# Optimization experiments

Hardware: AMD Instinct MI355X
Metric: run time of the kernel (lower is better)

Reference implementation:

```python
import jax, jax.numpy as jnp
import numpy as np

P = 50000      # number of graph nodes (cortical dipoles)
HID = 256      # hidden width
E = 800000     # number of nonzeros in Ahat (avg degree 16)


def setup_inputs() -> dict:
    key = jax.random.key(0)
    ks = jax.random.split(key, 12)
    beta = jax.random.normal(ks[0], (P, 1), dtype=jnp.float32)
    degree = jax.random.uniform(ks[1], (P, 1), dtype=jnp.float32)
    A_rows = jax.random.randint(ks[2], (E,), 0, P, dtype=jnp.int32)
    A_cols = jax.random.randint(ks[3], (E,), 0, P, dtype=jnp.int32)
    # normalized-adjacency-like positive values
    A_vals = jax.random.uniform(ks[4], (E,), dtype=jnp.float32) * (1.0 / 16.0)
    # parameters (torch nn.Linear stores weight as [out, in])
    s_in = 1.0 / np.sqrt(3.0)
    s_h = 1.0 / np.sqrt(HID)
    W_in = jax.random.uniform(ks[5], (HID, 3), jnp.float32, -s_in, s_in)
    b_in = jax.random.uniform(ks[6], (HID,), jnp.float32, -s_in, s_in)
    W_mp1 = jax.random.uniform(ks[7], (HID, HID), jnp.float32, -s_h, s_h)
    W_mp2 = jax.random.uniform(ks[8], (HID, HID), jnp.float32, -s_h, s_h)
    W_out = jax.random.uniform(ks[9], (1, HID), jnp.float32, -s_h, s_h)
    b_out = jax.random.uniform(ks[10], (1,), jnp.float32, -s_h, s_h)
    return {
        "beta": beta, "degree": degree,
        "A_rows": A_rows, "A_cols": A_cols, "A_vals": A_vals,
        "W_in": W_in, "b_in": b_in,
        "W_mp1": W_mp1, "W_mp2": W_mp2,
        "W_out": W_out, "b_out": b_out,
    }


def _spmm(A_rows, A_cols, A_vals, X):
    # sparse [P,P] @ dense [P,H] via gather + segment-sum over COO edges
    msgs = A_vals[:, None] * X[A_cols]            # [E, H]
    return jax.ops.segment_sum(msgs, A_rows, num_segments=P)


def reference(beta, degree, A_rows, A_cols, A_vals,
              W_in, b_in, W_mp1, W_mp2, W_out, b_out):
    x = jnp.concatenate([beta, beta ** 2, degree], axis=1)   # [P, 3]
    h = jax.nn.relu(x @ W_in.T + b_in)                       # [P, HID]
    AH = _spmm(A_rows, A_cols, A_vals, h)                    # one-hop
    A2H = _spmm(A_rows, A_cols, A_vals, AH)                  # two-hop
    h = jax.nn.relu(AH @ W_mp1.T + A2H @ W_mp2.T)            # fused sum + relu
    g = jax.nn.softplus(h @ W_out.T + b_out)                 # [P, 1]
    return g
```

## Files before the change

kernel.cpp:

```cpp
#include <hip/hip_runtime.h>
#include <math.h>

#define NP 50000
#define HIDDEN 256
#define NE 800000
#define CAP 64

#define OFF_X2     0ULL
#define OFF_BP     51200000ULL
#define OFF_CNT    51462144ULL
#define OFF_PC     51662144ULL
#define OFF_EV     52062144ULL

typedef __attribute__((ext_vector_type(8))) short bf16x8;
typedef __attribute__((ext_vector_type(8))) unsigned short u16x8;
typedef __attribute__((ext_vector_type(4))) float f32x4;

__device__ inline unsigned short f2bf(float f) {
    union { float f; unsigned int u; } x; x.f = f;
    unsigned int r = x.u + 0x7FFFu + ((x.u >> 16) & 1u);
    return (unsigned short)(r >> 16);
}
__device__ inline float bf2f(unsigned short u) {
    union { unsigned int u; float f; } x; x.u = ((unsigned int)u) << 16; return x.f;
}

__global__ void bp_kernel(const float* __restrict__ W1,
                          const float* __restrict__ W2,
                          unsigned short* __restrict__ Bp) {
    int t = blockIdx.x * 256 + threadIdx.x;
    int j = t >> 9;
    int k = t & 511;
    float v = (k < 256) ? W1[j * 256 + k] : W2[j * 256 + (k - 256)];
    Bp[(k >> 3) * 2048 + j * 8 + (k & 7)] = f2bf(v);
}

__global__ void pc_kernel(const float* __restrict__ beta,
                          const float* __restrict__ degree,
                          float2* __restrict__ pc) {
    int i = blockIdx.x * 256 + threadIdx.x;
    if (i < NP) pc[i] = make_float2(beta[i], degree[i]);
}

__global__ void scatter_ell(const int* __restrict__ rows,
                            const int* __restrict__ cols,
                            const float* __restrict__ vals,
                            int* __restrict__ cnt,
                            int2* __restrict__ ev) {
    int e = blockIdx.x * 256 + threadIdx.x;
    if (e < NE) {
        int r = rows[e];
        int pos = atomicAdd(&cnt[r], 1);
        if (pos < CAP)
            ev[(size_t)r * CAP + pos] = make_int2(cols[e], __float_as_int(vals[e]));
    }
}

__global__ __launch_bounds__(256) void spmm_embed_kernel(
        const int* __restrict__ cnt, const int2* __restrict__ ev,
        const float2* __restrict__ pc,
        const float* __restrict__ W_in, const float* __restrict__ b_in,
        unsigned short* __restrict__ Y, int ystride) {
    int w = threadIdx.x >> 6;
    int lane = threadIdx.x & 63;
    int r = blockIdx.x * 4 + w;
    if (r >= NP) return;
    int half = lane >> 5;
    int fo = (lane & 31) * 8;

    int n = min(cnt[r], CAP);
    int2 e2 = make_int2(0, 0);
    if (lane < n) e2 = ev[(size_t)r * CAP + lane];
    int col_l = e2.x;
    float val_l = __int_as_float(e2.y);

    float wr0[8], wr1[8], wr2[8], br[8];
    #pragma unroll
    for (int j = 0; j < 8; ++j) {
        wr0[j] = W_in[(fo + j) * 3 + 0];
        wr1[j] = W_in[(fo + j) * 3 + 1];
        wr2[j] = W_in[(fo + j) * 3 + 2];
        br[j]  = b_in[fo + j];
    }

    float acc[8] = {0.f,0.f,0.f,0.f,0.f,0.f,0.f,0.f};
    for (int i = 0; i < n; i += 8) {
        float2 p[4]; float vv[4];
        #pragma unroll
        for (int k = 0; k < 4; ++k) {
            int e = i + 2 * k + half;
            int es = (e < n) ? e : 0;
            int c = __shfl(col_l, es);
            vv[k] = __shfl(val_l, es);
            if (e >= n) vv[k] = 0.f;
            p[k] = pc[c];
        }
        #pragma unroll
        for (int k = 0; k < 4; ++k) {
            float b = p[k].x, d = p[k].y, v = vv[k];
            float b2 = b * b;
            #pragma unroll
            for (int j = 0; j < 8; ++j) {
                float t = fmaf(b, wr0[j], fmaf(b2, wr1[j], fmaf(d, wr2[j], br[j])));
                acc[j] = fmaf(v, fmaxf(t, 0.f), acc[j]);
            }
        }
    }
    #pragma unroll
    for (int j = 0; j < 8; ++j) acc[j] += __shfl_xor(acc[j], 32);
    if (half == 0) {
        u16x8 o;
        #pragma unroll
        for (int j = 0; j < 8; ++j) o[j] = f2bf(acc[j]);
        *reinterpret_cast<u16x8*>(Y + (size_t)r * ystride + fo) = o;
    }
}

__global__ __launch_bounds__(256) void spmm_gather_kernel(
        const int* __restrict__ cnt, const int2* __restrict__ ev,
        const unsigned short* __restrict__ X, int xstride,
        unsigned short* __restrict__ Y, int ystride) {
    int w = threadIdx.x >> 6;
    int lane = threadIdx.x & 63;
    int r = blockIdx.x * 4 + w;
    if (r >= NP) return;
    int half = lane >> 5;
    int fo = (lane & 31) * 8;

    int n = min(cnt[r], CAP);
    int2 e2 = make_int2(0, 0);
    if (lane < n) e2 = ev[(size_t)r * CAP + lane];
    int col_l = e2.x;
    float val_l = __int_as_float(e2.y);

    float acc[8] = {0.f,0.f,0.f,0.f,0.f,0.f,0.f,0.f};
    for (int i = 0; i < n; i += 8) {
        int cc[4]; float vv[4];
        #pragma unroll
        for (int k = 0; k < 4; ++k) {
            int e = i + 2 * k + half;
            int es = (e < n) ? e : 0;
            cc[k] = __shfl(col_l, es);
            vv[k] = __shfl(val_l, es);
            if (e >= n) vv[k] = 0.f;
        }
        u16x8 x0 = *reinterpret_cast<const u16x8*>(X + (size_t)cc[0] * xstride + fo);
        u16x8 x1 = *reinterpret_cast<const u16x8*>(X + (size_t)cc[1] * xstride + fo);
        u16x8 x2 = *reinterpret_cast<const u16x8*>(X + (size_t)cc[2] * xstride + fo);
        u16x8 x3 = *reinterpret_cast<const u16x8*>(X + (size_t)cc[3] * xstride + fo);
        #pragma unroll
        for (int j = 0; j < 8; ++j) acc[j] = fmaf(vv[0], bf2f(x0[j]), acc[j]);
        #pragma unroll
        for (int j = 0; j < 8; ++j) acc[j] = fmaf(vv[1], bf2f(x1[j]), acc[j]);
        #pragma unroll
        for (int j = 0; j < 8; ++j) acc[j] = fmaf(vv[2], bf2f(x2[j]), acc[j]);
        #pragma unroll
        for (int j = 0; j < 8; ++j) acc[j] = fmaf(vv[3], bf2f(x3[j]), acc[j]);
    }
    #pragma unroll
    for (int j = 0; j < 8; ++j) acc[j] += __shfl_xor(acc[j], 32);
    if (half == 0) {
        u16x8 o;
        #pragma unroll
        for (int j = 0; j < 8; ++j) o[j] = f2bf(acc[j]);
        *reinterpret_cast<u16x8*>(Y + (size_t)r * ystride + fo) = o;
    }
}

__global__ __launch_bounds__(512, 4) void mp_out_kernel(
        const unsigned short* __restrict__ X2,
        const unsigned short* __restrict__ Bp,
        const float* __restrict__ W_out, const float* __restrict__ b_out,
        float* __restrict__ g) {
    __shared__ unsigned short As[128 * 64];
    __shared__ unsigned short Bs[8 * 256 * 8];
    __shared__ float Ps[4][128];

    int tid = threadIdx.x;
    int w = tid >> 6;
    int lane = tid & 63;
    int wr = w >> 2;
    int wc = w & 3;
    int p0 = blockIdx.x * 128;

    f32x4 acc[4][4];
    #pragma unroll
    for (int i = 0; i < 4; ++i)
        #pragma unroll
        for (int j = 0; j < 4; ++j)
            acc[i][j] = (f32x4){0.f, 0.f, 0.f, 0.f};

    for (int kc = 0; kc < 8; ++kc) {
        __syncthreads();
        #pragma unroll
        for (int it = 0; it < 2; ++it) {
            int slot = it * 512 + tid;
            int ss = slot ^ ((slot >> 3) & 7);
            int row = ss >> 3;
            int ko = (ss & 7) * 8;
            int grow = p0 + row;
            if (grow >= NP) grow = NP - 1;
            float4 v = *reinterpret_cast<const float4*>(X2 + (size_t)grow * 512 + kc * 64 + ko);
            *reinterpret_cast<float4*>(&As[slot * 8]) = v;
        }
        #pragma unroll
        for (int it = 0; it < 4; ++it) {
            int c2 = it * 512 + tid;
            float4 v = *reinterpret_cast<const float4*>(
                Bp + ((size_t)(kc * 8 + (c2 >> 8))) * 2048 + (c2 & 255) * 8);
            *reinterpret_cast<float4*>(&Bs[c2 * 8]) = v;
        }
        __syncthreads();
        #pragma unroll
        for (int ks = 0; ks < 2; ++ks) {
            bf16x8 af[4], bfr[4];
            #pragma unroll
            for (int rt = 0; rt < 4; ++rt) {
                int row = wr * 64 + rt * 16 + (lane & 15);
                int elem = row * 64 + ks * 32 + (lane >> 4) * 8;
                elem ^= (row & 7) << 3;
                af[rt] = *reinterpret_cast<const bf16x8*>(&As[elem]);
            }
            #pragma unroll
            for (int nt = 0; nt < 4; ++nt) {
                int col = wc * 64 + nt * 16 + (lane & 15);
                int kbl = ks * 4 + (lane >> 4);
                bfr[nt] = *reinterpret_cast<const bf16x8*>(&Bs[kbl * 2048 + col * 8]);
            }
            #pragma unroll
            for (int rt = 0; rt < 4; ++rt)
                #pragma unroll
                for (int nt = 0; nt < 4; ++nt)
                    acc[rt][nt] = __builtin_amdgcn_mfma_f32_16x16x32_bf16(
                        af[rt], bfr[nt], acc[rt][nt], 0, 0, 0);
        }
    }

    float wv[4];
    #pragma unroll
    for (int nt = 0; nt < 4; ++nt)
        wv[nt] = W_out[wc * 64 + nt * 16 + (lane & 15)];

    float ps[4][4];
    #pragma unroll
    for (int rt = 0; rt < 4; ++rt)
        #pragma unroll
        for (int r = 0; r < 4; ++r) {
            float s = 0.f;
            #pragma unroll
            for (int nt = 0; nt < 4; ++nt)
                s = fmaf(fmaxf(acc[rt][nt][r], 0.0f), wv[nt], s);
            ps[rt][r] = s;
        }
    #pragma unroll
    for (int m = 1; m < 16; m <<= 1)
        #pragma unroll
        for (int rt = 0; rt < 4; ++rt)
            #pragma unroll
            for (int r = 0; r < 4; ++r)
                ps[rt][r] += __shfl_xor(ps[rt][r], m);

    if ((lane & 15) == 0) {
        int rb = wr * 64 + (lane >> 4) * 4;
        #pragma unroll
        for (int rt = 0; rt < 4; ++rt)
            #pragma unroll
            for (int r = 0; r < 4; ++r)
                Ps[wc][rb + rt * 16 + r] = ps[rt][r];
    }
    __syncthreads();
    if (tid < 128) {
        int p = p0 + tid;
        if (p < NP) {
            float z = Ps[0][tid] + Ps[1][tid] + Ps[2][tid] + Ps[3][tid] + b_out[0];
            g[p] = fmaxf(z, 0.0f) + log1pf(expf(-fabsf(z)));
        }
    }
}

extern "C" void kernel_launch(void* const* d_in, const int* in_sizes, int n_in,
                              void* d_out, int out_size, void* d_ws, size_t ws_size,
                              hipStream_t stream) {
    const float* beta   = (const float*)d_in[0];
    const float* degree = (const float*)d_in[1];
    const int*   A_rows = (const int*)d_in[2];
    const int*   A_cols = (const int*)d_in[3];
    const float* A_vals = (const float*)d_in[4];
    const float* W_in   = (const float*)d_in[5];
    const float* b_in   = (const float*)d_in[6];
    const float* W_mp1  = (const float*)d_in[7];
    const float* W_mp2  = (const float*)d_in[8];
    const float* W_out  = (const float*)d_in[9];
    const float* b_out  = (const float*)d_in[10];
    float* g = (float*)d_out;

    char* ws = (char*)d_ws;
    unsigned short* X2 = (unsigned short*)(ws + OFF_X2);
    unsigned short* Bp = (unsigned short*)(ws + OFF_BP);
    int*    cnt = (int*)(ws + OFF_CNT);
    float2* pc  = (float2*)(ws + OFF_PC);
    int2*   ev  = (int2*)(ws + OFF_EV);

    hipMemsetAsync(cnt, 0, NP * sizeof(int), stream);

    bp_kernel<<<512, 256, 0, stream>>>(W_mp1, W_mp2, Bp);
    pc_kernel<<<(NP + 255) / 256, 256, 0, stream>>>(beta, degree, pc);

    scatter_ell<<<(NE + 255) / 256, 256, 0, stream>>>(A_rows, A_cols, A_vals, cnt, ev);

    spmm_embed_kernel<<<(NP + 3) / 4, 256, 0, stream>>>(cnt, ev, pc, W_in, b_in,
                                                        X2, 512);
    spmm_gather_kernel<<<(NP + 3) / 4, 256, 0, stream>>>(cnt, ev, X2, 512,
                                                         X2 + 256, 512);

    mp_out_kernel<<<(NP + 127) / 128, 512, 0, stream>>>(X2, Bp, W_out, b_out, g);
}
```

Measured before the change: 176.2 us.

## Split AH/A2H into dense buffers and deepen SpMM gather loop unrolling

The interleaved [P,512] bf16 buffer becomes two contiguous [P,256] buffers, AH and A2H, so each gathered row of the second SpMM sits in a compact array with better cache density. The embed and gather SpMM loops now issue 8 gathers per step, with tail steps of 4 and 2, and no per-edge bounds masking, to raise memory-level parallelism. The tail relies on lanes past n holding zero col/val from the initial ev load. The GEMM kernel selects its source buffer per K chunk.

```diff
diff --git a/kernel.cpp b/kernel.cpp
--- a/kernel.cpp
+++ b/kernel.cpp
@@ -6,7 +6,8 @@
 #define NE 800000
 #define CAP 64
 
-#define OFF_X2     0ULL
+#define OFF_AH     0ULL
+#define OFF_A2H    25600000ULL
 #define OFF_BP     51200000ULL
 #define OFF_CNT    51462144ULL
 #define OFF_PC     51662144ULL
@@ -60,7 +61,7 @@
         const int* __restrict__ cnt, const int2* __restrict__ ev,
         const float2* __restrict__ pc,
         const float* __restrict__ W_in, const float* __restrict__ b_in,
-        unsigned short* __restrict__ Y, int ystride) {
+        unsigned short* __restrict__ Y) {
     int w = threadIdx.x >> 6;
     int lane = threadIdx.x & 63;
     int r = blockIdx.x * 4 + w;
@@ -84,42 +85,50 @@
     }
 
     float acc[8] = {0.f,0.f,0.f,0.f,0.f,0.f,0.f,0.f};
-    for (int i = 0; i < n; i += 8) {
-        float2 p[4]; float vv[4];
-        #pragma unroll
-        for (int k = 0; k < 4; ++k) {
-            int e = i + 2 * k + half;
-            int es = (e < n) ? e : 0;
-            int c = __shfl(col_l, es);
-            vv[k] = __shfl(val_l, es);
-            if (e >= n) vv[k] = 0.f;
-            p[k] = pc[c];
-        }
-        #pragma unroll
-        for (int k = 0; k < 4; ++k) {
-            float b = p[k].x, d = p[k].y, v = vv[k];
-            float b2 = b * b;
-            #pragma unroll
-            for (int j = 0; j < 8; ++j) {
-                float t = fmaf(b, wr0[j], fmaf(b2, wr1[j], fmaf(d, wr2[j], br[j])));
-                acc[j] = fmaf(v, fmaxf(t, 0.f), acc[j]);
-            }
-        }
-    }
+
+#define ESTEP(d)                                                             \
+    {                                                                        \
+        float2 pr[d]; float vr[d];                                           \
+        _Pragma("unroll")                                                    \
+        for (int k = 0; k < (d); ++k) {                                      \
+            int e = i + 2 * k + half;                                        \
+            int c = __shfl(col_l, e);                                        \
+            vr[k] = __shfl(val_l, e);                                        \
+            pr[k] = pc[c];                                                   \
+        }                                                                    \
+        _Pragma("unroll")                                                    \
+        for (int k = 0; k < (d); ++k) {                                      \
+            float b = pr[k].x, dd = pr[k].y, v = vr[k];                      \
+            float b2 = b * b;                                                \
+            _Pragma("unroll")                                                \
+            for (int j = 0; j < 8; ++j) {                                    \
+                float t = fmaf(b, wr0[j], fmaf(b2, wr1[j], fmaf(dd, wr2[j], br[j]))); \
+                acc[j] = fmaf(v, fmaxf(t, 0.f), acc[j]);                     \
+            }                                                                \
+        }                                                                    \
+    }
+
+    int i = 0;
+    for (; i + 16 <= n; i += 16) ESTEP(8)
+    if (i + 8 <= n) { ESTEP(4) i += 8; }
+    if (i + 4 <= n) { ESTEP(2) i += 4; }
+    if (i < n)      { ESTEP(2) }
+#undef ESTEP
+
     #pragma unroll
     for (int j = 0; j < 8; ++j) acc[j] += __shfl_xor(acc[j], 32);
     if (half == 0) {
         u16x8 o;
         #pragma unroll
         for (int j = 0; j < 8; ++j) o[j] = f2bf(acc[j]);
-        *reinterpret_cast<u16x8*>(Y + (size_t)r * ystride + fo) = o;
+        *reinterpret_cast<u16x8*>(Y + (size_t)r * HIDDEN + fo) = o;
     }
 }
 
 __global__ __launch_bounds__(256) void spmm_gather_kernel(
         const int* __restrict__ cnt, const int2* __restrict__ ev,
-        const unsigned short* __restrict__ X, int xstride,
-        unsigned short* __restrict__ Y, int ystride) {
+        const unsigned short* __restrict__ X,
+        unsigned short* __restrict__ Y) {
     int w = threadIdx.x >> 6;
     int lane = threadIdx.x & 63;
     int r = blockIdx.x * 4 + w;
@@ -134,41 +143,44 @@
     float val_l = __int_as_float(e2.y);
 
     float acc[8] = {0.f,0.f,0.f,0.f,0.f,0.f,0.f,0.f};
-    for (int i = 0; i < n; i += 8) {
-        int cc[4]; float vv[4];
-        #pragma unroll
-        for (int k = 0; k < 4; ++k) {
-            int e = i + 2 * k + half;
-            int es = (e < n) ? e : 0;
-            cc[k] = __shfl(col_l, es);
-            vv[k] = __shfl(val_l, es);
-            if (e >= n) vv[k] = 0.f;
-        }
-        u16x8 x0 = *reinterpret_cast<const u16x8*>(X + (size_t)cc[0] * xstride + fo);
-        u16x8 x1 = *reinterpret_cast<const u16x8*>(X + (size_t)cc[1] * xstride + fo);
-        u16x8 x2 = *reinterpret_cast<const u16x8*>(X + (size_t)cc[2] * xstride + fo);
-        u16x8 x3 = *reinterpret_cast<const u16x8*>(X + (size_t)cc[3] * xstride + fo);
-        #pragma unroll
-        for (int j = 0; j < 8; ++j) acc[j] = fmaf(vv[0], bf2f(x0[j]), acc[j]);
-        #pragma unroll
-        for (int j = 0; j < 8; ++j) acc[j] = fmaf(vv[1], bf2f(x1[j]), acc[j]);
-        #pragma unroll
-        for (int j = 0; j < 8; ++j) acc[j] = fmaf(vv[2], bf2f(x2[j]), acc[j]);
-        #pragma unroll
-        for (int j = 0; j < 8; ++j) acc[j] = fmaf(vv[3], bf2f(x3[j]), acc[j]);
-    }
+
+#define GSTEP(d)                                                             \
+    {                                                                        \
+        u16x8 xr[d]; float vr[d];                                            \
+        _Pragma("unroll")                                                    \
+        for (int k = 0; k < (d); ++k) {                                      \
+            int e = i + 2 * k + half;                                        \
+            int c = __shfl(col_l, e);                                        \
+            vr[k] = __shfl(val_l, e);                                        \
+            xr[k] = *reinterpret_cast<const u16x8*>(X + (size_t)c * HIDDEN + fo); \
+        }                                                                    \
+        _Pragma("unroll")                                                    \
+        for (int k = 0; k < (d); ++k)                                        \
+            _Pragma("unroll")                                                \
+            for (int j = 0; j < 8; ++j)                                      \
+                acc[j] = fmaf(vr[k], bf2f(xr[k][j]), acc[j]);                \
+    }
+
+    int i = 0;
+    for (; i + 16 <= n; i += 16) GSTEP(8)
+    if (i + 8 <= n) { GSTEP(4) i += 8; }
+    if (i + 4 <= n) { GSTEP(2) i += 4; }
+    if (i < n)      { GSTEP(2) }
+#undef GSTEP
+
     #pragma unroll
     for (int j = 0; j < 8; ++j) acc[j] += __shfl_xor(acc[j], 32);
     if (half == 0) {
         u16x8 o;
         #pragma unroll
         for (int j = 0; j < 8; ++j) o[j] = f2bf(acc[j]);
-        *reinterpret_cast<u16x8*>(Y + (size_t)r * ystride + fo) = o;
+        *reinterpret_cast<u16x8*>(Y + (size_t)r * HIDDEN + fo) = o;
     }
 }
 
 __global__ __launch_bounds__(512, 4) void mp_out_kernel(
-        const unsigned short* __restrict__ X2,
+        const unsigned short* __restrict__ AH,
+        const unsigned short* __restrict__ A2H,
         const unsigned short* __restrict__ Bp,
         const float* __restrict__ W_out, const float* __restrict__ b_out,
         float* __restrict__ g) {
@@ -191,6 +203,8 @@
             acc[i][j] = (f32x4){0.f, 0.f, 0.f, 0.f};
 
     for (int kc = 0; kc < 8; ++kc) {
+        const unsigned short* Xsrc = (kc < 4) ? AH : A2H;
+        int k0 = (kc & 3) * 64;
         __syncthreads();
         #pragma unroll
         for (int it = 0; it < 2; ++it) {
@@ -200,7 +214,7 @@
             int ko = (ss & 7) * 8;
             int grow = p0 + row;
             if (grow >= NP) grow = NP - 1;
-            float4 v = *reinterpret_cast<const float4*>(X2 + (size_t)grow * 512 + kc * 64 + ko);
+            float4 v = *reinterpret_cast<const float4*>(Xsrc + (size_t)grow * HIDDEN + k0 + ko);
             *reinterpret_cast<float4*>(&As[slot * 8]) = v;
         }
         #pragma unroll
@@ -295,8 +309,9 @@
     float* g = (float*)d_out;
 
     char* ws = (char*)d_ws;
-    unsigned short* X2 = (unsigned short*)(ws + OFF_X2);
-    unsigned short* Bp = (unsigned short*)(ws + OFF_BP);
+    unsigned short* AH  = (unsigned short*)(ws + OFF_AH);
+    unsigned short* A2H = (unsigned short*)(ws + OFF_A2H);
+    unsigned short* Bp  = (unsigned short*)(ws + OFF_BP);
     int*    cnt = (int*)(ws + OFF_CNT);
     float2* pc  = (float2*)(ws + OFF_PC);
     int2*   ev  = (int2*)(ws + OFF_EV);
@@ -308,10 +323,8 @@
 
     scatter_ell<<<(NE + 255) / 256, 256, 0, stream>>>(A_rows, A_cols, A_vals, cnt, ev);
 
-    spmm_embed_kernel<<<(NP + 3) / 4, 256, 0, stream>>>(cnt, ev, pc, W_in, b_in,
-                                                        X2, 512);
-    spmm_gather_kernel<<<(NP + 3) / 4, 256, 0, stream>>>(cnt, ev, X2, 512,
-                                                         X2 + 256, 512);
-
-    mp_out_kernel<<<(NP + 127) / 128, 512, 0, stream>>>(X2, Bp, W_out, b_out, g);
-}
+    spmm_embed_kernel<<<(NP + 3) / 4, 256, 0, stream>>>(cnt, ev, pc, W_in, b_in, AH);
+    spmm_gather_kernel<<<(NP + 3) / 4, 256, 0, stream>>>(cnt, ev, AH, A2H);
+
+    mp_out_kernel<<<(NP + 127) / 128, 512, 0, stream>>>(AH, A2H, Bp, W_out, b_out, g);
+}
```

New measurement: 175.2 us. No clear change (-0.5%).
